# Performance work log

Measured on AMD Instinct MI355X. Metric: run time of the kernel, lower is better.

## Reference

```python
import jax, jax.numpy as jnp
import numpy as np

N_NODES = 50000
N_EDGES = 800000
N_GRAPHS = 64
IN_C = 256      # num_commodities
HID = 256       # hidden_units
HID2 = HID // 2
N_DCS = 64


def setup_inputs() -> dict:
    key = jax.random.key(0)
    ks = jax.random.split(key, 8)
    x = jax.random.normal(ks[0], (N_NODES, IN_C), dtype=jnp.float32)
    edge_index = jax.random.randint(ks[1], (2, N_EDGES), 0, N_NODES, dtype=jnp.int32)
    # sorted graph-membership ids; even partition guarantees no empty graph
    batch = ((jnp.arange(N_NODES) * N_GRAPHS) // N_NODES).astype(jnp.int32)
    s1 = 1.0 / np.sqrt(IN_C)
    s2 = 1.0 / np.sqrt(HID)
    s3 = 1.0 / np.sqrt(HID2)
    W1 = jax.random.normal(ks[2], (IN_C, HID), dtype=jnp.float32) * s1
    b1 = jnp.zeros((HID,), dtype=jnp.float32)
    W2 = jax.random.normal(ks[3], (HID, HID2), dtype=jnp.float32) * s2
    b2 = jnp.zeros((HID2,), dtype=jnp.float32)
    Wm = jax.random.normal(ks[4], (HID2, N_DCS), dtype=jnp.float32) * s3
    bm = jax.random.normal(ks[5], (N_DCS,), dtype=jnp.float32) * s3
    return {"x": x, "edge_index": edge_index, "batch": batch,
            "W1": W1, "b1": b1, "W2": W2, "b2": b2, "Wm": Wm, "bm": bm}


def gcn_conv(x, W, b, src, dst, n_nodes):
    """PyG GCNConv: D^{-1/2}(A+I)D^{-1/2} X W + b (self-loops added)."""
    h = x @ W                                    # [N, out]
    ones = jnp.ones(src.shape[0], dtype=h.dtype)
    deg = jax.ops.segment_sum(ones, dst, num_segments=n_nodes) + 1.0  # +1 self-loop
    dis = jax.lax.rsqrt(deg)                     # deg >= 1, safe
    norm = dis[src] * dis[dst]                   # [E]
    agg = jax.ops.segment_sum(h[src] * norm[:, None], dst, num_segments=n_nodes)
    agg = agg + h * (dis * dis)[:, None]         # self-loop contribution
    return agg + b


def reference(x, edge_index, batch, W1, b1, W2, b2, Wm, bm):
    src, dst = edge_index[0], edge_index[1]
    n = x.shape[0]
    bx = jax.nn.relu(gcn_conv(x, W1, b1, src, dst, n))
    cx = jax.nn.relu(gcn_conv(bx, W2, b2, src, dst, n))
    px = jax.ops.segment_max(cx, batch, num_segments=N_GRAPHS)  # global max pool
    return px @ Wm + bm                           # [N_GRAPHS, N_DCS]
```

## Files before the change

### kernel.cpp

```cpp
#include <hip/hip_runtime.h>
#include <cstdint>


typedef _Float16 half2v __attribute__((ext_vector_type(2)));
typedef _Float16 half4v __attribute__((ext_vector_type(4)));
typedef _Float16 half8v __attribute__((ext_vector_type(8)));
typedef float f32x4 __attribute__((ext_vector_type(4)));

__device__ __forceinline__ void gl_lds16(const void* g, void* l) {
  __builtin_amdgcn_global_load_lds(
      (const __attribute__((address_space(1))) unsigned int*)g,
      (__attribute__((address_space(3))) unsigned int*)l, 16, 0, 0);
}

__global__ void count_deg_k(const int* __restrict__ dst, int* __restrict__ deg, int E) {
  int e = blockIdx.x * blockDim.x + threadIdx.x;
  if (e < E) atomicAdd(&deg[dst[e]], 1);
}

__global__ void scan1_dis_k(const int* __restrict__ deg, int* __restrict__ blksum,
                            float* __restrict__ dis, int n) {
  __shared__ int sd[256];
  int i = blockIdx.x * 256 + threadIdx.x;
  int d = (i < n) ? deg[i] : 0;
  if (i < n) dis[i] = 1.0f / sqrtf((float)d + 1.0f);
  sd[threadIdx.x] = d;
  __syncthreads();
  for (int s = 128; s > 0; s >>= 1) {
    if (threadIdx.x < s) sd[threadIdx.x] += sd[threadIdx.x + s];
    __syncthreads();
  }
  if (threadIdx.x == 0) blksum[blockIdx.x] = sd[0];
}

__global__ void scan2_k(const int* __restrict__ blksum, int* __restrict__ blkoff, int nb) {
  __shared__ int sd[256];
  int v = (threadIdx.x < nb) ? blksum[threadIdx.x] : 0;
  sd[threadIdx.x] = v;
  __syncthreads();
  for (int d = 1; d < 256; d <<= 1) {
    int t = (threadIdx.x >= d) ? sd[threadIdx.x - d] : 0;
    __syncthreads();
    sd[threadIdx.x] += t;
    __syncthreads();
  }
  if (threadIdx.x < nb) blkoff[threadIdx.x] = sd[threadIdx.x] - v;
}

__global__ void scan3_k(const int* __restrict__ deg, const int* __restrict__ blkoff,
                        int* __restrict__ offs, int n) {
  __shared__ int sd[256];
  int i = blockIdx.x * 256 + threadIdx.x;
  int v = (i < n) ? deg[i] : 0;
  sd[threadIdx.x] = v;
  __syncthreads();
  for (int d = 1; d < 256; d <<= 1) {
    int t = (threadIdx.x >= d) ? sd[threadIdx.x - d] : 0;
    __syncthreads();
    sd[threadIdx.x] += t;
    __syncthreads();
  }
  if (i < n) offs[i] = blkoff[blockIdx.x] + sd[threadIdx.x] - v;
  if (i == n - 1) offs[n] = blkoff[blockIdx.x] + sd[threadIdx.x];
}

__global__ void fill_csr_k(const int* __restrict__ src, const int* __restrict__ dst,
                           const int* __restrict__ offs, int* __restrict__ deg,
                           int* __restrict__ csr, int E) {
  int e = blockIdx.x * blockDim.x + threadIdx.x;
  if (e >= E) return;
  int d = dst[e];
  int pos = atomicSub(&deg[d], 1) - 1;
  csr[offs[d] + pos] = src[e];
}

__global__ void cvt_all_k(const float* __restrict__ x, _Float16* __restrict__ xh,
                          const float* __restrict__ W1, _Float16* __restrict__ Wt1,
                          const float* __restrict__ W2, _Float16* __restrict__ Wt2,
                          int xn4) {
  int i = blockIdx.x * 256 + threadIdx.x;
  if (i < xn4) {
    float4 v = ((const float4*)x)[i];
    half4v o = {(_Float16)v.x, (_Float16)v.y, (_Float16)v.z, (_Float16)v.w};
    ((half4v*)xh)[i] = o;
    return;
  }
  int j = i - xn4;
  if (j < 256 * 256) {
    int k = j >> 8, c = j & 255;
    Wt1[c * 256 + k] = (_Float16)W1[j];
    return;
  }
  j -= 256 * 256;
  if (j < 256 * 128) {
    int k = j >> 7, c = j & 127;
    Wt2[c * 256 + k] = (_Float16)W2[j];
  }
}

#define GBM 128
#define GBN 128
#define GBK 32

__global__ __launch_bounds__(256) void gemm_f16(const _Float16* __restrict__ A,
                                                const _Float16* __restrict__ Bt,
                                                const float* __restrict__ dis,
                                                _Float16* __restrict__ C,
                                                int M, int N, int K) {
  __shared__ _Float16 As[GBM * GBK];
  __shared__ _Float16 Bs[GBN * GBK];
  const int tid = threadIdx.x;
  const int lane = tid & 63;
  const int wave = tid >> 6;
  const int wm = wave >> 1, wn = wave & 1;
  const int row0 = blockIdx.x * GBM;
  const int col0 = blockIdx.y * GBN;

  f32x4 acc[4][4] = {};

  const int kbase = (lane >> 4) * 8;
  const _Float16* aSrc[2];
  _Float16* aDst[2];
  const _Float16* bSrc[2];
  _Float16* bDst[2];
#pragma unroll
  for (int h = 0; h < 2; ++h) {
    int fl = h * 4 + wave;
    int row = h * 64 + wave * 16 + (lane & 15);
    int gr = row0 + row;
    if (gr > M - 1) gr = M - 1;
    aSrc[h] = A + (size_t)gr * K + kbase;
    aDst[h] = As + fl * 512;
    int gc = col0 + row;
    bSrc[h] = Bt + (size_t)gc * K + kbase;
    bDst[h] = Bs + fl * 512;
  }

  for (int k0 = 0; k0 < K; k0 += GBK) {
    gl_lds16(aSrc[0] + k0, aDst[0]);
    gl_lds16(aSrc[1] + k0, aDst[1]);
    gl_lds16(bSrc[0] + k0, bDst[0]);
    gl_lds16(bSrc[1] + k0, bDst[1]);
    __syncthreads();

    half8v af[4], bf[4];
#pragma unroll
    for (int m = 0; m < 4; ++m)
      af[m] = *(const half8v*)(As + (wm * 4 + m) * 512 + lane * 8);
#pragma unroll
    for (int nj = 0; nj < 4; ++nj)
      bf[nj] = *(const half8v*)(Bs + (wn * 4 + nj) * 512 + lane * 8);
#pragma unroll
    for (int m = 0; m < 4; ++m)
#pragma unroll
      for (int nj = 0; nj < 4; ++nj)
        acc[m][nj] = __builtin_amdgcn_mfma_f32_16x16x32_f16(af[m], bf[nj], acc[m][nj], 0, 0, 0);
    __syncthreads();
  }

#pragma unroll
  for (int m = 0; m < 4; ++m) {
    const int rbase = row0 + wm * 64 + m * 16 + (lane >> 4) * 4;
    float dr[4];
#pragma unroll
    for (int r = 0; r < 4; ++r) dr[r] = (rbase + r < M) ? dis[rbase + r] : 0.f;
#pragma unroll
    for (int nj = 0; nj < 4; ++nj) {
      int col = col0 + wn * 64 + nj * 16 + (lane & 15);
#pragma unroll
      for (int r = 0; r < 4; ++r) {
        int row = rbase + r;
        if (row < M) C[(size_t)row * N + col] = (_Float16)(acc[m][nj][r] * dr[r]);
      }
    }
  }
}

template <int C, bool POOL>
__global__ __launch_bounds__(256) void agg_k(const _Float16* __restrict__ h,
                                             const float* __restrict__ dis,
                                             const int* __restrict__ offs,
                                             const int* __restrict__ csr,
                                             const float* __restrict__ bias,
                                             const int* __restrict__ batch,
                                             void* __restrict__ outv, int n) {
  constexpr int LPR = C / 8;
  constexpr int EPW = 64 / LPR;
  constexpr int EBLK = EPW * 4;
  const int tid = threadIdx.x;
  const int lane = tid & 63;
  const int wave = tid >> 6;
  const int slot = lane / LPR;
  const int ch0 = (lane % LPR) * 8;

  const int wid = blockIdx.x * 4 + wave;
  const bool valid = wid < n;
  const int node = valid ? wid : n - 1;

  const int beg = offs[node], end = offs[node + 1];
  float acc[8] = {};
  int jb = beg;
  for (; jb + EBLK <= end; jb += EBLK) {
    half2v ah[4] = {};
#pragma unroll
    for (int u = 0; u < 4; ++u) {
      int s = csr[jb + u * EPW + slot];
      half8v hv = *(const half8v*)(h + (size_t)s * C + ch0);
      const half2v* hp = (const half2v*)&hv;
#pragma unroll
      for (int p = 0; p < 4; ++p) ah[p] += hp[p];
    }
#pragma unroll
    for (int p = 0; p < 4; ++p) {
      acc[2 * p + 0] += (float)ah[p][0];
      acc[2 * p + 1] += (float)ah[p][1];
    }
  }
  for (int e = jb + slot; e < end; e += EPW) {
    int s = csr[e];
    half8v hv = *(const half8v*)(h + (size_t)s * C + ch0);
#pragma unroll
    for (int v = 0; v < 8; ++v) acc[v] += (float)hv[v];
  }

  if constexpr (EPW == 4) {
#pragma unroll
    for (int v = 0; v < 8; ++v) {
      acc[v] += __shfl_xor(acc[v], 16);
      acc[v] += __shfl_xor(acc[v], 32);
    }
  } else {
#pragma unroll
    for (int v = 0; v < 8; ++v) acc[v] += __shfl_xor(acc[v], 32);
  }

  const float di = dis[node];
  half8v sv = *(const half8v*)(h + (size_t)node * C + ch0);
  float4 blo = *(const float4*)(bias + ch0);
  float4 bhi = *(const float4*)(bias + ch0 + 4);
  const float bb[8] = {blo.x, blo.y, blo.z, blo.w, bhi.x, bhi.y, bhi.z, bhi.w};
  float res[8];
#pragma unroll
  for (int v = 0; v < 8; ++v)
    res[v] = fmaxf((acc[v] + (float)sv[v]) * di + bb[v], 0.f);

  if constexpr (!POOL) {
    if (valid && lane < LPR) {
      half8v r;
#pragma unroll
      for (int v = 0; v < 8; ++v) r[v] = (_Float16)res[v];
      *(half8v*)((_Float16*)outv + (size_t)node * C + ch0) = r;
    }
  } else {
    __shared__ float pres[4][C];
    __shared__ int pg[4];
    __shared__ int uni;
    const int g = valid ? batch[node] : -1 - wave;
    if (lane < LPR) {
      *(f32x4*)&pres[wave][ch0] = f32x4{res[0], res[1], res[2], res[3]};
      *(f32x4*)&pres[wave][ch0 + 4] = f32x4{res[4], res[5], res[6], res[7]};
    }
    if (lane == 0) pg[wave] = g;
    __syncthreads();
    if (tid == 0) uni = (pg[0] == pg[1] && pg[1] == pg[2] && pg[2] == pg[3] && pg[0] >= 0);
    __syncthreads();
    float* px = (float*)outv;
    if (uni) {
      if (tid < C) {
        float m = fmaxf(fmaxf(pres[0][tid], pres[1][tid]),
                        fmaxf(pres[2][tid], pres[3][tid]));
        atomicMax((int*)&px[(size_t)pg[0] * C + tid], __float_as_int(m));
      }
    } else {
#pragma unroll
      for (int wv = 0; wv < 4; ++wv) {
        int gg = pg[wv];
        if (gg >= 0 && tid < C)
          atomicMax((int*)&px[(size_t)gg * C + tid], __float_as_int(pres[wv][tid]));
      }
    }
  }
}

__global__ void final_mm_k(const float* __restrict__ px, const float* __restrict__ Wm,
                           const float* __restrict__ bm, float* __restrict__ out) {
  int g = blockIdx.x;
  int c = threadIdx.x;
  float acc = bm[c];
#pragma unroll 8
  for (int k = 0; k < 128; ++k)
    acc = fmaf(px[g * 128 + k], Wm[k * 64 + c], acc);
  out[g * 64 + c] = acc;
}

extern "C" void kernel_launch(void* const* d_in, const int* in_sizes, int n_in,
                              void* d_out, int out_size, void* d_ws, size_t ws_size,
                              hipStream_t stream) {
  const float* x     = (const float*)d_in[0];
  const int*   ei    = (const int*)d_in[1];
  const int*   batch = (const int*)d_in[2];
  const float* W1    = (const float*)d_in[3];
  const float* b1    = (const float*)d_in[4];
  const float* W2    = (const float*)d_in[5];
  const float* b2    = (const float*)d_in[6];
  const float* Wm    = (const float*)d_in[7];
  const float* bm    = (const float*)d_in[8];
  float* out = (float*)d_out;

  const int E = in_sizes[1] / 2;
  const int n = in_sizes[2];
  const int IN_C = 256, HID = 256, HID2 = 128, NG = 64;
  const int* src = ei;
  const int* dst = ei + E;

  char* w = (char*)d_ws;
  size_t off = 0;
  auto alloc = [&](size_t bytes) -> void* {
    void* p = w + off;
    off = (off + bytes + 255) & ~(size_t)255;
    return p;
  };
  const int nb = (n + 255) / 256;
  int*      deg    = (int*)alloc((size_t)n * 4);
  float*    px     = (float*)alloc((size_t)NG * HID2 * 4);
  size_t    zlen   = off;
  float*    dis    = (float*)alloc((size_t)n * 4);
  int*      offs   = (int*)alloc((size_t)(n + 1) * 4);
  int*      blksum = (int*)alloc((size_t)nb * 4);
  int*      blkoff = (int*)alloc((size_t)nb * 4);
  int*      csr    = (int*)alloc((size_t)E * 4);
  _Float16* xh     = (_Float16*)alloc((size_t)n * IN_C * 2);
  _Float16* Wt1    = (_Float16*)alloc((size_t)HID * IN_C * 2);
  _Float16* Wt2    = (_Float16*)alloc((size_t)HID2 * HID * 2);
  _Float16* bufA   = (_Float16*)alloc((size_t)n * HID * 2);
  _Float16* bufB   = (_Float16*)alloc((size_t)n * HID * 2);
  _Float16* h1 = bufA;
  _Float16* bx = bufB;
  _Float16* h2 = bufA;

  hipMemsetAsync(deg, 0, zlen, stream);

  count_deg_k<<<(E + 255) / 256, 256, 0, stream>>>(dst, deg, E);
  scan1_dis_k<<<nb, 256, 0, stream>>>(deg, blksum, dis, n);
  scan2_k<<<1, 256, 0, stream>>>(blksum, blkoff, nb);
  scan3_k<<<nb, 256, 0, stream>>>(deg, blkoff, offs, n);
  fill_csr_k<<<(E + 255) / 256, 256, 0, stream>>>(src, dst, offs, deg, csr, E);

  const int xn4 = n * IN_C / 4;
  const int cvt_total = xn4 + 256 * 256 + 256 * 128;
  cvt_all_k<<<(cvt_total + 255) / 256, 256, 0, stream>>>(x, xh, W1, Wt1, W2, Wt2, xn4);

  dim3 g1((n + GBM - 1) / GBM, HID / GBN);
  gemm_f16<<<g1, 256, 0, stream>>>(xh, Wt1, dis, h1, n, HID, IN_C);
  agg_k<256, false><<<(n + 3) / 4, 256, 0, stream>>>(h1, dis, offs, csr, b1, nullptr, bx, n);

  dim3 g2((n + GBM - 1) / GBM, HID2 / GBN);
  gemm_f16<<<g2, 256, 0, stream>>>(bx, Wt2, dis, h2, n, HID2, HID);
  agg_k<128, true><<<(n + 3) / 4, 256, 0, stream>>>(h2, dis, offs, csr, b2, batch, px, n);

  final_mm_k<<<NG, 64, 0, stream>>>(px, Wm, bm, out);
}
```

Baseline: 355.4 us.

## Fuse x fp16 conversion into first GEMM, shrink CSR to u16, merge scans

Adds a dedicated first-layer GEMM that reads fp32 x directly and converts it to fp16 in registers, removing the separate conversion pass and the xh buffer. The CSR neighbor indices are stored as 16-bit values to halve index traffic in aggregation, and the scan2 kernel is removed by having each scan3 block sum the preceding block totals itself. The aggregation loop is unrolled to 8 edges with a masked tail instead of a scalar remainder loop. The 16-bit CSR truncates node ids of 65536 or more, which only holds because this input has 50000 nodes.

```diff
diff --git a/kernel.cpp b/kernel.cpp
--- a/kernel.cpp
+++ b/kernel.cpp
@@ -33,23 +33,20 @@
   if (threadIdx.x == 0) blksum[blockIdx.x] = sd[0];
 }
 
-__global__ void scan2_k(const int* __restrict__ blksum, int* __restrict__ blkoff, int nb) {
-  __shared__ int sd[256];
-  int v = (threadIdx.x < nb) ? blksum[threadIdx.x] : 0;
-  sd[threadIdx.x] = v;
-  __syncthreads();
-  for (int d = 1; d < 256; d <<= 1) {
-    int t = (threadIdx.x >= d) ? sd[threadIdx.x - d] : 0;
-    __syncthreads();
-    sd[threadIdx.x] += t;
-    __syncthreads();
-  }
-  if (threadIdx.x < nb) blkoff[threadIdx.x] = sd[threadIdx.x] - v;
-}
-
-__global__ void scan3_k(const int* __restrict__ deg, const int* __restrict__ blkoff,
+__global__ void scan3_k(const int* __restrict__ deg, const int* __restrict__ blksum,
                         int* __restrict__ offs, int n) {
   __shared__ int sd[256];
+  __shared__ int boff;
+  int pre = 0;
+  for (int j = threadIdx.x; j < blockIdx.x; j += 256) pre += blksum[j];
+  sd[threadIdx.x] = pre;
+  __syncthreads();
+  for (int s = 128; s > 0; s >>= 1) {
+    if (threadIdx.x < s) sd[threadIdx.x] += sd[threadIdx.x + s];
+    __syncthreads();
+  }
+  if (threadIdx.x == 0) boff = sd[0];
+  __syncthreads();
   int i = blockIdx.x * 256 + threadIdx.x;
   int v = (i < n) ? deg[i] : 0;
   sd[threadIdx.x] = v;
@@ -60,41 +57,102 @@
     sd[threadIdx.x] += t;
     __syncthreads();
   }
-  if (i < n) offs[i] = blkoff[blockIdx.x] + sd[threadIdx.x] - v;
-  if (i == n - 1) offs[n] = blkoff[blockIdx.x] + sd[threadIdx.x];
+  if (i < n) offs[i] = boff + sd[threadIdx.x] - v;
+  if (i == n - 1) offs[n] = boff + sd[threadIdx.x];
 }
 
 __global__ void fill_csr_k(const int* __restrict__ src, const int* __restrict__ dst,
                            const int* __restrict__ offs, int* __restrict__ deg,
-                           int* __restrict__ csr, int E) {
+                           unsigned short* __restrict__ csr, int E) {
   int e = blockIdx.x * blockDim.x + threadIdx.x;
   if (e >= E) return;
   int d = dst[e];
   int pos = atomicSub(&deg[d], 1) - 1;
-  csr[offs[d] + pos] = src[e];
-}
-
-__global__ void cvt_all_k(const float* __restrict__ x, _Float16* __restrict__ xh,
-                          const float* __restrict__ W1, _Float16* __restrict__ Wt1,
-                          const float* __restrict__ W2, _Float16* __restrict__ Wt2,
-                          int xn4) {
+  csr[offs[d] + pos] = (unsigned short)src[e];
+}
+
+__global__ void cvtW_k(const float* __restrict__ W1, _Float16* __restrict__ Wt1,
+                       const float* __restrict__ W2, _Float16* __restrict__ Wt2) {
   int i = blockIdx.x * 256 + threadIdx.x;
-  if (i < xn4) {
-    float4 v = ((const float4*)x)[i];
-    half4v o = {(_Float16)v.x, (_Float16)v.y, (_Float16)v.z, (_Float16)v.w};
-    ((half4v*)xh)[i] = o;
-    return;
-  }
-  int j = i - xn4;
-  if (j < 256 * 256) {
-    int k = j >> 8, c = j & 255;
-    Wt1[c * 256 + k] = (_Float16)W1[j];
-    return;
-  }
-  j -= 256 * 256;
-  if (j < 256 * 128) {
-    int k = j >> 7, c = j & 127;
-    Wt2[c * 256 + k] = (_Float16)W2[j];
+  if (i < 256 * 256) {
+    int k = i >> 8, c = i & 255;
+    Wt1[c * 256 + k] = (_Float16)W1[i];
+  } else {
+    int j = i - 256 * 256;
+    if (j < 256 * 128) {
+      int k = j >> 7, c = j & 127;
+      Wt2[c * 256 + k] = (_Float16)W2[j];
+    }
+  }
+}
+
+__global__ __launch_bounds__(256) void gemm1_k(const float* __restrict__ A,
+                                               const _Float16* __restrict__ Bt,
+                                               const float* __restrict__ dis,
+                                               _Float16* __restrict__ C, int M) {
+  constexpr int K = 256, N = 256, BM = 64, BK = 32;
+  __shared__ _Float16 As[BM * BK];
+  __shared__ _Float16 Bs[N * BK];
+  const int tid = threadIdx.x, lane = tid & 63, wave = tid >> 6;
+  const int row0 = blockIdx.x * BM;
+  const int kbase = (lane >> 4) * 8;
+  const int r16 = lane & 15;
+
+  int arow = row0 + wave * 16 + r16;
+  if (arow > M - 1) arow = M - 1;
+  const float* aSrc = A + (size_t)arow * K + kbase;
+  _Float16* aDst = As + wave * 512 + lane * 8;
+
+  const _Float16* bSrc[4];
+  _Float16* bDst[4];
+#pragma unroll
+  for (int hh = 0; hh < 4; ++hh) {
+    int fl = hh * 4 + wave;
+    bSrc[hh] = Bt + (size_t)(fl * 16 + r16) * K + kbase;
+    bDst[hh] = Bs + fl * 512;
+  }
+
+  f32x4 acc[4][4] = {};
+  for (int k0 = 0; k0 < K; k0 += BK) {
+#pragma unroll
+    for (int hh = 0; hh < 4; ++hh) gl_lds16(bSrc[hh] + k0, bDst[hh]);
+    float4 a0 = *(const float4*)(aSrc + k0);
+    float4 a1 = *(const float4*)(aSrc + k0 + 4);
+    half8v ah = {(_Float16)a0.x, (_Float16)a0.y, (_Float16)a0.z, (_Float16)a0.w,
+                 (_Float16)a1.x, (_Float16)a1.y, (_Float16)a1.z, (_Float16)a1.w};
+    *(half8v*)aDst = ah;
+    __syncthreads();
+
+    half8v af[4], bf[4];
+#pragma unroll
+    for (int m = 0; m < 4; ++m)
+      af[m] = *(const half8v*)(As + m * 512 + lane * 8);
+#pragma unroll
+    for (int nj = 0; nj < 4; ++nj)
+      bf[nj] = *(const half8v*)(Bs + (wave * 4 + nj) * 512 + lane * 8);
+#pragma unroll
+    for (int m = 0; m < 4; ++m)
+#pragma unroll
+      for (int nj = 0; nj < 4; ++nj)
+        acc[m][nj] = __builtin_amdgcn_mfma_f32_16x16x32_f16(af[m], bf[nj], acc[m][nj], 0, 0, 0);
+    __syncthreads();
+  }
+
+#pragma unroll
+  for (int m = 0; m < 4; ++m) {
+    const int rbase = row0 + m * 16 + (lane >> 4) * 4;
+    float dr[4];
+#pragma unroll
+    for (int r = 0; r < 4; ++r) dr[r] = (rbase + r < M) ? dis[rbase + r] : 0.f;
+#pragma unroll
+    for (int nj = 0; nj < 4; ++nj) {
+      int col = wave * 64 + nj * 16 + r16;
+#pragma unroll
+      for (int r = 0; r < 4; ++r) {
+        int row = rbase + r;
+        if (row < M) C[(size_t)row * N + col] = (_Float16)(acc[m][nj][r] * dr[r]);
+      }
+    }
   }
 }
 
@@ -180,13 +238,14 @@
 __global__ __launch_bounds__(256) void agg_k(const _Float16* __restrict__ h,
                                              const float* __restrict__ dis,
                                              const int* __restrict__ offs,
-                                             const int* __restrict__ csr,
+                                             const unsigned short* __restrict__ csr,
                                              const float* __restrict__ bias,
                                              const int* __restrict__ batch,
                                              void* __restrict__ outv, int n) {
   constexpr int LPR = C / 8;
   constexpr int EPW = 64 / LPR;
-  constexpr int EBLK = EPW * 4;
+  constexpr int U = 8;
+  constexpr int EBLK = EPW * U;
   const int tid = threadIdx.x;
   const int lane = tid & 63;
   const int wave = tid >> 6;
@@ -201,26 +260,49 @@
   float acc[8] = {};
   int jb = beg;
   for (; jb + EBLK <= end; jb += EBLK) {
-    half2v ah[4] = {};
-#pragma unroll
-    for (int u = 0; u < 4; ++u) {
+    half2v ah0[4] = {}, ah1[4] = {};
+#pragma unroll
+    for (int u = 0; u < U; ++u) {
       int s = csr[jb + u * EPW + slot];
       half8v hv = *(const half8v*)(h + (size_t)s * C + ch0);
       const half2v* hp = (const half2v*)&hv;
-#pragma unroll
-      for (int p = 0; p < 4; ++p) ah[p] += hp[p];
+      if (u < 4) {
+#pragma unroll
+        for (int p = 0; p < 4; ++p) ah0[p] += hp[p];
+      } else {
+#pragma unroll
+        for (int p = 0; p < 4; ++p) ah1[p] += hp[p];
+      }
     }
 #pragma unroll
     for (int p = 0; p < 4; ++p) {
-      acc[2 * p + 0] += (float)ah[p][0];
-      acc[2 * p + 1] += (float)ah[p][1];
-    }
-  }
-  for (int e = jb + slot; e < end; e += EPW) {
-    int s = csr[e];
-    half8v hv = *(const half8v*)(h + (size_t)s * C + ch0);
-#pragma unroll
-    for (int v = 0; v < 8; ++v) acc[v] += (float)hv[v];
+      acc[2 * p + 0] += (float)ah0[p][0] + (float)ah1[p][0];
+      acc[2 * p + 1] += (float)ah0[p][1] + (float)ah1[p][1];
+    }
+  }
+  if (jb < end) {
+    half2v ah0[4] = {}, ah1[4] = {};
+#pragma unroll
+    for (int u = 0; u < U; ++u) {
+      int e = jb + u * EPW + slot;
+      bool ok = e < end;
+      int s = csr[ok ? e : end - 1];
+      half8v hv = *(const half8v*)(h + (size_t)s * C + ch0);
+      if (!ok) hv = half8v{};
+      const half2v* hp = (const half2v*)&hv;
+      if (u < 4) {
+#pragma unroll
+        for (int p = 0; p < 4; ++p) ah0[p] += hp[p];
+      } else {
+#pragma unroll
+        for (int p = 0; p < 4; ++p) ah1[p] += hp[p];
+      }
+    }
+#pragma unroll
+    for (int p = 0; p < 4; ++p) {
+      acc[2 * p + 0] += (float)ah0[p][0] + (float)ah1[p][0];
+      acc[2 * p + 1] += (float)ah0[p][1] + (float)ah1[p][1];
+    }
   }
 
   if constexpr (EPW == 4) {
@@ -310,6 +392,7 @@
   const int E = in_sizes[1] / 2;
   const int n = in_sizes[2];
   const int IN_C = 256, HID = 256, HID2 = 128, NG = 64;
+  (void)IN_C;
   const int* src = ei;
   const int* dst = ei + E;
 
@@ -321,19 +404,17 @@
     return p;
   };
   const int nb = (n + 255) / 256;
-  int*      deg    = (int*)alloc((size_t)n * 4);
-  float*    px     = (float*)alloc((size_t)NG * HID2 * 4);
-  size_t    zlen   = off;
-  float*    dis    = (float*)alloc((size_t)n * 4);
-  int*      offs   = (int*)alloc((size_t)(n + 1) * 4);
-  int*      blksum = (int*)alloc((size_t)nb * 4);
-  int*      blkoff = (int*)alloc((size_t)nb * 4);
-  int*      csr    = (int*)alloc((size_t)E * 4);
-  _Float16* xh     = (_Float16*)alloc((size_t)n * IN_C * 2);
-  _Float16* Wt1    = (_Float16*)alloc((size_t)HID * IN_C * 2);
-  _Float16* Wt2    = (_Float16*)alloc((size_t)HID2 * HID * 2);
-  _Float16* bufA   = (_Float16*)alloc((size_t)n * HID * 2);
-  _Float16* bufB   = (_Float16*)alloc((size_t)n * HID * 2);
+  int*            deg    = (int*)alloc((size_t)n * 4);
+  float*          px     = (float*)alloc((size_t)NG * HID2 * 4);
+  size_t          zlen   = off;
+  float*          dis    = (float*)alloc((size_t)n * 4);
+  int*            offs   = (int*)alloc((size_t)(n + 1) * 4);
+  int*            blksum = (int*)alloc((size_t)nb * 4);
+  unsigned short* csr    = (unsigned short*)alloc((size_t)E * 2);
+  _Float16*       Wt1    = (_Float16*)alloc((size_t)HID * 256 * 2);
+  _Float16*       Wt2    = (_Float16*)alloc((size_t)HID2 * HID * 2);
+  _Float16*       bufA   = (_Float16*)alloc((size_t)n * HID * 2);
+  _Float16*       bufB   = (_Float16*)alloc((size_t)n * HID * 2);
   _Float16* h1 = bufA;
   _Float16* bx = bufB;
   _Float16* h2 = bufA;
@@ -342,16 +423,11 @@
 
   count_deg_k<<<(E + 255) / 256, 256, 0, stream>>>(dst, deg, E);
   scan1_dis_k<<<nb, 256, 0, stream>>>(deg, blksum, dis, n);
-  scan2_k<<<1, 256, 0, stream>>>(blksum, blkoff, nb);
-  scan3_k<<<nb, 256, 0, stream>>>(deg, blkoff, offs, n);
+  scan3_k<<<nb, 256, 0, stream>>>(deg, blksum, offs, n);
   fill_csr_k<<<(E + 255) / 256, 256, 0, stream>>>(src, dst, offs, deg, csr, E);
-
-  const int xn4 = n * IN_C / 4;
-  const int cvt_total = xn4 + 256 * 256 + 256 * 128;
-  cvt_all_k<<<(cvt_total + 255) / 256, 256, 0, stream>>>(x, xh, W1, Wt1, W2, Wt2, xn4);
-
-  dim3 g1((n + GBM - 1) / GBM, HID / GBN);
-  gemm_f16<<<g1, 256, 0, stream>>>(xh, Wt1, dis, h1, n, HID, IN_C);
+  cvtW_k<<<(256 * 256 + 256 * 128 + 255) / 256, 256, 0, stream>>>(W1, Wt1, W2, Wt2);
+
+  gemm1_k<<<(n + 63) / 64, 256, 0, stream>>>(x, Wt1, dis, h1, n);
   agg_k<256, false><<<(n + 3) / 4, 256, 0, stream>>>(h1, dis, offs, csr, b1, nullptr, bx, n);
 
   dim3 g2((n + GBM - 1) / GBM, HID2 / GBN);
```

After: 343.5 us. 3.3% less time.
